# Performance work log

Measured on AMD Instinct MI355X. Metric: run time of the kernel, lower is better.

The kernel has to match this reference:

```python
import jax, jax.numpy as jnp
import numpy as np
from jax import lax

# Dims (match init_kwargs)
NP, DP = 32, 8      # num_primary_a, dim_primary_a
NT, DT = 16, 16     # num_timecaps_a, dim_timecaps
KT = 3              # kernel_timecaps_a
EPS = 1e-7


def setup_inputs() -> dict:
    key = jax.random.key(0)
    k1, k2, k3 = jax.random.split(key, 3)
    B, T = 8, 1024
    x = jax.random.normal(k1, (B, T, NP, DP), dtype=jnp.float32)
    # Conv2D kernel: HWIO = [kernel_t, dim_primary_a, in_ch=1, out_ch=NT*DT]
    conv_kernel = jax.random.normal(k2, (KT, DP, 1, NT * DT), dtype=jnp.float32) * 0.05
    conv_bias = jnp.zeros((NT * DT,), dtype=jnp.float32)
    B_weight = jax.random.normal(k3, (T, NT, 1, NP), dtype=jnp.float32) * 0.05
    return {"x": x, "conv_kernel": conv_kernel, "conv_bias": conv_bias, "B_weight": B_weight}


def reference(x, conv_kernel, conv_bias, B_weight):
    B, T, Np, Dp = x.shape
    # reshape1: [B, T, Np*Dp, 1]
    xr = x.reshape(B, T, Np * Dp, 1)
    # Conv2D(filters=NT*DT, kernel=[KT, Dp], strides=[1, Dp], padding='same', relu)
    y = lax.conv_general_dilated(
        xr, conv_kernel,
        window_strides=(1, Dp), padding='SAME',
        dimension_numbers=('NHWC', 'HWIO', 'NHWC'))
    y = jax.nn.relu(y + conv_bias)  # [B, T, Np, NT*DT]
    # reshape2 + permute -> U_hat: [B, T, NT, Np, DT]
    U = y.reshape(B, T, Np, NT, DT).transpose(0, 1, 3, 2, 4)
    # self-similarity attention
    A = jnp.einsum('btnpd,btnqd->btnpq', U, U) / jnp.sqrt(jnp.float32(Dp))
    C = jax.nn.softmax(A.sum(axis=-2, keepdims=True), axis=-1)  # [B,T,NT,1,Np]
    out = jnp.einsum('btnop,btnpd->btnod', C + B_weight, U)  # [B,T,NT,1,DT]
    out = out[..., 0, :]  # squeeze axis=-2 -> [B,T,NT,DT]
    # squash
    norm = jnp.linalg.norm(out, axis=-1, keepdims=True)
    sq = norm * norm
    return (sq / (sq + 1.0)) * (out / (norm + EPS))
```

## Files before the change

### kernel.cpp

```cpp
#include <hip/hip_runtime.h>

#define T_DIM 1024

typedef short short8 __attribute__((ext_vector_type(8)));
typedef float f32x4  __attribute__((ext_vector_type(4)));

__device__ __forceinline__ unsigned pk_bf16(float lo, float hi) {
    unsigned r;
    asm("v_cvt_pk_bf16_f32 %0, %1, %2" : "=v"(r) : "v"(lo), "v"(hi));
    return r;
}

__global__ void kpack_kernel(const float* __restrict__ K,
                             const float* __restrict__ bias,
                             uint4* __restrict__ Kp) {
    const int kb  = blockIdx.x;
    const int col = threadIdx.x;
    uint4 wv = make_uint4(0u, 0u, 0u, 0u);
    if (kb < 3) {
        const float* kp = K + kb * 8 * 256 + col;
        wv.x = pk_bf16(kp[0 * 256], kp[1 * 256]);
        wv.y = pk_bf16(kp[2 * 256], kp[3 * 256]);
        wv.z = pk_bf16(kp[4 * 256], kp[5 * 256]);
        wv.w = pk_bf16(kp[6 * 256], kp[7 * 256]);
    } else {
        wv.x = pk_bf16(bias[col], 0.f);
    }
    Kp[kb * 256 + col] = wv;
}

__device__ __forceinline__ void allred_add16_x4(float& a, float& b, float& c, float& d) {
    asm volatile(
        "s_nop 1\n\t"
        "v_add_f32_dpp %0,%0,%0 row_ror:8 row_mask:0xf bank_mask:0xf\n\t"
        "v_add_f32_dpp %1,%1,%1 row_ror:8 row_mask:0xf bank_mask:0xf\n\t"
        "v_add_f32_dpp %2,%2,%2 row_ror:8 row_mask:0xf bank_mask:0xf\n\t"
        "v_add_f32_dpp %3,%3,%3 row_ror:8 row_mask:0xf bank_mask:0xf\n\t"
        "v_add_f32_dpp %0,%0,%0 row_ror:4 row_mask:0xf bank_mask:0xf\n\t"
        "v_add_f32_dpp %1,%1,%1 row_ror:4 row_mask:0xf bank_mask:0xf\n\t"
        "v_add_f32_dpp %2,%2,%2 row_ror:4 row_mask:0xf bank_mask:0xf\n\t"
        "v_add_f32_dpp %3,%3,%3 row_ror:4 row_mask:0xf bank_mask:0xf\n\t"
        "v_add_f32_dpp %0,%0,%0 row_ror:2 row_mask:0xf bank_mask:0xf\n\t"
        "v_add_f32_dpp %1,%1,%1 row_ror:2 row_mask:0xf bank_mask:0xf\n\t"
        "v_add_f32_dpp %2,%2,%2 row_ror:2 row_mask:0xf bank_mask:0xf\n\t"
        "v_add_f32_dpp %3,%3,%3 row_ror:2 row_mask:0xf bank_mask:0xf\n\t"
        "v_add_f32_dpp %0,%0,%0 row_ror:1 row_mask:0xf bank_mask:0xf\n\t"
        "v_add_f32_dpp %1,%1,%1 row_ror:1 row_mask:0xf bank_mask:0xf\n\t"
        "v_add_f32_dpp %2,%2,%2 row_ror:1 row_mask:0xf bank_mask:0xf\n\t"
        "v_add_f32_dpp %3,%3,%3 row_ror:1 row_mask:0xf bank_mask:0xf"
        : "+v"(a), "+v"(b), "+v"(c), "+v"(d));
}
__device__ __forceinline__ void allred_add16_v4(f32x4& v) {
    float a = v[0], b = v[1], c = v[2], d = v[3];
    allred_add16_x4(a, b, c, d);
    v = (f32x4){a, b, c, d};
}
__device__ __forceinline__ float allred_add16_s(float v) {
    asm volatile(
        "s_nop 1\n\t"
        "v_add_f32_dpp %0,%0,%0 row_ror:8 row_mask:0xf bank_mask:0xf\n\t"
        "s_nop 1\n\t"
        "v_add_f32_dpp %0,%0,%0 row_ror:4 row_mask:0xf bank_mask:0xf\n\t"
        "s_nop 1\n\t"
        "v_add_f32_dpp %0,%0,%0 row_ror:2 row_mask:0xf bank_mask:0xf\n\t"
        "s_nop 1\n\t"
        "v_add_f32_dpp %0,%0,%0 row_ror:1 row_mask:0xf bank_mask:0xf"
        : "+v"(v));
    return v;
}

__device__ __forceinline__ void wave_ds_fence() {
    asm volatile("s_waitcnt lgkmcnt(0)" ::: "memory");
}

template <int CODE>
__device__ __forceinline__ float swz_xor(float v) {
    return __int_as_float(__builtin_amdgcn_ds_swizzle(__float_as_int(v), CODE));
}

#define USTRIDE 260

__global__ __launch_bounds__(256, 4) void caps_kernel(
    const float* __restrict__ x,
    const float* __restrict__ Bw,
    const uint4* __restrict__ Kp,
    float* __restrict__ out)
{
    const int bt  = blockIdx.x;
    const int t   = bt & (T_DIM - 1);
    const int tid = threadIdx.x;
    const int l   = tid & 63;
    const int w   = tid >> 6;
    const int kb  = l >> 4;
    const int r16 = l & 15;
    const int n   = tid >> 4, j = tid & 15;

    __shared__ float Urow[32 * USTRIDE];

    const float bwj0 = Bw[(size_t)t * 512 + n * 32 + j];
    const float bwj1 = Bw[(size_t)t * 512 + n * 32 + 16 + j];

    short8 bx[2];
    if (kb == 3) {
        union { short8 s; uint4 u; } one;
        one.u = make_uint4(0x00003F80u, 0u, 0u, 0u);
        bx[0] = bx[1] = one.s;
    } else {
        const int  tt    = t + kb - 1;
        const bool valid = (tt >= 0) && (tt < T_DIM);
        #pragma unroll
        for (int qt = 0; qt < 2; ++qt) {
            float4 x0 = make_float4(0.f, 0.f, 0.f, 0.f), x1 = x0;
            if (valid) {
                const float* xp = x + ((size_t)(bt + kb - 1) * 256 + (qt * 16 + r16) * 8);
                x0 = *reinterpret_cast<const float4*>(xp);
                x1 = *reinterpret_cast<const float4*>(xp + 4);
            }
            union { short8 s; uint4 u; } bu;
            bu.u.x = pk_bf16(x0.x, x0.y);
            bu.u.y = pk_bf16(x0.z, x0.w);
            bu.u.z = pk_bf16(x1.x, x1.y);
            bu.u.w = pk_bf16(x1.z, x1.w);
            bx[qt] = bu.s;
        }
    }

    short8 af[4];
    #pragma unroll
    for (int oti = 0; oti < 4; ++oti) {
        union { short8 s; uint4 u; } au;
        au.u = Kp[kb * 256 + w * 64 + oti * 16 + r16];
        af[oti] = au.s;
    }

    const f32x4 z = (f32x4){0.f, 0.f, 0.f, 0.f};
    f32x4 acc[2][4];
    #pragma unroll
    for (int qt = 0; qt < 2; ++qt)
        #pragma unroll
        for (int oti = 0; oti < 4; ++oti)
            acc[qt][oti] = __builtin_amdgcn_mfma_f32_16x16x32_bf16(
                af[oti], bx[qt], z, 0, 0, 0);

    float* wbase = &Urow[r16 * USTRIDE + w * 64 + kb * 4];
    #pragma unroll
    for (int qt = 0; qt < 2; ++qt)
        #pragma unroll
        for (int oti = 0; oti < 4; ++oti) {
            f32x4 uv;
            #pragma unroll
            for (int e = 0; e < 4; ++e)
                uv[e] = fmaxf(acc[qt][oti][e], 0.f);
            *reinterpret_cast<f32x4*>(&wbase[qt * 16 * USTRIDE + oti * 16]) = uv;
        }

    wave_ds_fence();

    const float* rbase = &Urow[j * USTRIDE + n * 16];
    f32x4 r0[4], r1[4];
    #pragma unroll
    for (int i = 0; i < 4; ++i) {
        r0[i] = *reinterpret_cast<const f32x4*>(&rbase[4 * i]);
        r1[i] = *reinterpret_cast<const f32x4*>(&rbase[16 * USTRIDE + 4 * i]);
    }

    f32x4 V[4];
    #pragma unroll
    for (int i = 0; i < 4; ++i) {
        V[i] = r0[i] + r1[i];
        allred_add16_v4(V[i]);
    }

    float s0 = 0.f, s1 = 0.f;
    #pragma unroll
    for (int i = 0; i < 4; ++i)
        #pragma unroll
        for (int c = 0; c < 4; ++c) {
            s0 = fmaf(V[i][c], r0[i][c], s0);
            s1 = fmaf(V[i][c], r1[i][c], s1);
        }

    const float C2 = 0.51011597846f;
    const float e0 = exp2f(s0 * C2), e1 = exp2f(s1 * C2);
    const float es = allred_add16_s(e0 + e1);
    const float inv = __builtin_amdgcn_rcpf(es);
    const float c0 = fmaf(e0, inv, bwj0);
    const float c1 = fmaf(e1, inv, bwj1);

    float op16[16];
    #pragma unroll
    for (int i = 0; i < 4; ++i)
        #pragma unroll
        for (int c = 0; c < 4; ++c)
            op16[4 * i + c] = fmaf(c0, r0[i][c], c1 * r1[i][c]);

    float v8[8];
    #pragma unroll
    for (int s = 0; s < 8; ++s) {
        const float keep = (j & 8) ? op16[s + 8] : op16[s];
        const float send = (j & 8) ? op16[s] : op16[s + 8];
        v8[s] = keep + swz_xor<0x201F>(send);
    }
    float v4[4];
    #pragma unroll
    for (int s = 0; s < 4; ++s) {
        const float keep = (j & 4) ? v4[0] * 0.f + ((j & 4) ? v8[s + 4] : v8[s]) : v8[s];
        (void)keep;
        const float kp = (j & 4) ? v8[s + 4] : v8[s];
        const float sd = (j & 4) ? v8[s] : v8[s + 4];
        v4[s] = kp + swz_xor<0x101F>(sd);
    }
    float v2[2];
    #pragma unroll
    for (int s = 0; s < 2; ++s) {
        const float kp = (j & 2) ? v4[s + 2] : v4[s];
        const float sd = (j & 2) ? v4[s] : v4[s + 2];
        v2[s] = kp + swz_xor<0x081F>(sd);
    }
    const float kp1 = (j & 1) ? v2[1] : v2[0];
    const float sd1 = (j & 1) ? v2[0] : v2[1];
    const float ox = kp1 + swz_xor<0x041F>(sd1);

    const float ss  = allred_add16_s(ox * ox);
    const float nrm = sqrtf(ss);
    const float res = ss * __builtin_amdgcn_rcpf(ss + 1.f) *
                      (ox * __builtin_amdgcn_rcpf(nrm + 1e-7f));

    out[(size_t)bt * 256 + tid] = res;
}

extern "C" void kernel_launch(void* const* d_in, const int* in_sizes, int n_in,
                              void* d_out, int out_size, void* d_ws, size_t ws_size,
                              hipStream_t stream) {
    const float* x    = (const float*)d_in[0];
    const float* K    = (const float*)d_in[1];
    const float* bias = (const float*)d_in[2];
    const float* Bw   = (const float*)d_in[3];
    float* out        = (float*)d_out;
    uint4* Kp         = (uint4*)d_ws;

    kpack_kernel<<<4, 256, 0, stream>>>(K, bias, Kp);

    const int B  = in_sizes[0] / (T_DIM * 32 * 8);
    const int nb = B * T_DIM;
    caps_kernel<<<nb, 256, 0, stream>>>(x, Bw, Kp, out);
}
```

Baseline: 33.81 us.

## Fuse weight packing into caps kernel and compute column sums before LDS

Drops the separate kernel that packed conv weights to bf16 and has each block load and convert the fp32 weights itself, which removes one launch and the dependency between kernels. The column sum V is now computed right after the MFMA from the accumulators, using DPP reductions, and written to a small shared array instead of being recomputed from LDS reads by every thread. In exchange, each block performs redundant scalar global loads and conversions of the weights, which add load latency at kernel start. It also adds an extra shared buffer.

Measured after the change: 37.82 us. 11.8% more time.

```diff
diff --git a/kernel.cpp b/kernel.cpp
--- a/kernel.cpp
+++ b/kernel.cpp
@@ -9,24 +9,6 @@
     unsigned r;
     asm("v_cvt_pk_bf16_f32 %0, %1, %2" : "=v"(r) : "v"(lo), "v"(hi));
     return r;
-}
-
-__global__ void kpack_kernel(const float* __restrict__ K,
-                             const float* __restrict__ bias,
-                             uint4* __restrict__ Kp) {
-    const int kb  = blockIdx.x;
-    const int col = threadIdx.x;
-    uint4 wv = make_uint4(0u, 0u, 0u, 0u);
-    if (kb < 3) {
-        const float* kp = K + kb * 8 * 256 + col;
-        wv.x = pk_bf16(kp[0 * 256], kp[1 * 256]);
-        wv.y = pk_bf16(kp[2 * 256], kp[3 * 256]);
-        wv.z = pk_bf16(kp[4 * 256], kp[5 * 256]);
-        wv.w = pk_bf16(kp[6 * 256], kp[7 * 256]);
-    } else {
-        wv.x = pk_bf16(bias[col], 0.f);
-    }
-    Kp[kb * 256 + col] = wv;
 }
 
 __device__ __forceinline__ void allred_add16_x4(float& a, float& b, float& c, float& d) {
@@ -50,11 +32,6 @@
         "v_add_f32_dpp %3,%3,%3 row_ror:1 row_mask:0xf bank_mask:0xf"
         : "+v"(a), "+v"(b), "+v"(c), "+v"(d));
 }
-__device__ __forceinline__ void allred_add16_v4(f32x4& v) {
-    float a = v[0], b = v[1], c = v[2], d = v[3];
-    allred_add16_x4(a, b, c, d);
-    v = (f32x4){a, b, c, d};
-}
 __device__ __forceinline__ float allred_add16_s(float v) {
     asm volatile(
         "s_nop 1\n\t"
@@ -83,7 +60,8 @@
 __global__ __launch_bounds__(256, 4) void caps_kernel(
     const float* __restrict__ x,
     const float* __restrict__ Bw,
-    const uint4* __restrict__ Kp,
+    const float* __restrict__ K,
+    const float* __restrict__ bias,
     float* __restrict__ out)
 {
     const int bt  = blockIdx.x;
@@ -96,6 +74,7 @@
     const int n   = tid >> 4, j = tid & 15;
 
     __shared__ float Urow[32 * USTRIDE];
+    __shared__ float Vs[256];
 
     const float bwj0 = Bw[(size_t)t * 512 + n * 32 + j];
     const float bwj1 = Bw[(size_t)t * 512 + n * 32 + 16 + j];
@@ -128,8 +107,17 @@
     short8 af[4];
     #pragma unroll
     for (int oti = 0; oti < 4; ++oti) {
+        const int col = w * 64 + oti * 16 + r16;
         union { short8 s; uint4 u; } au;
-        au.u = Kp[kb * 256 + w * 64 + oti * 16 + r16];
+        if (kb < 3) {
+            const float* kp = K + (kb * 8) * 256 + col;
+            au.u.x = pk_bf16(kp[0 * 256], kp[1 * 256]);
+            au.u.y = pk_bf16(kp[2 * 256], kp[3 * 256]);
+            au.u.z = pk_bf16(kp[4 * 256], kp[5 * 256]);
+            au.u.w = pk_bf16(kp[6 * 256], kp[7 * 256]);
+        } else {
+            au.u = make_uint4(pk_bf16(bias[col], 0.f), 0u, 0u, 0u);
+        }
         af[oti] = au.s;
     }
 
@@ -144,31 +132,33 @@
 
     float* wbase = &Urow[r16 * USTRIDE + w * 64 + kb * 4];
     #pragma unroll
-    for (int qt = 0; qt < 2; ++qt)
-        #pragma unroll
-        for (int oti = 0; oti < 4; ++oti) {
-            f32x4 uv;
-            #pragma unroll
-            for (int e = 0; e < 4; ++e)
-                uv[e] = fmaxf(acc[qt][oti][e], 0.f);
-            *reinterpret_cast<f32x4*>(&wbase[qt * 16 * USTRIDE + oti * 16]) = uv;
-        }
+    for (int oti = 0; oti < 4; ++oti) {
+        f32x4 uv0, uv1;
+        #pragma unroll
+        for (int e = 0; e < 4; ++e) {
+            uv0[e] = fmaxf(acc[0][oti][e], 0.f);
+            uv1[e] = fmaxf(acc[1][oti][e], 0.f);
+        }
+        *reinterpret_cast<f32x4*>(&wbase[oti * 16]) = uv0;
+        *reinterpret_cast<f32x4*>(&wbase[16 * USTRIDE + oti * 16]) = uv1;
+
+        float v0 = uv0[0] + uv1[0], v1 = uv0[1] + uv1[1];
+        float v2 = uv0[2] + uv1[2], v3 = uv0[3] + uv1[3];
+        allred_add16_x4(v0, v1, v2, v3);
+        if (r16 == 0)
+            *reinterpret_cast<f32x4*>(&Vs[w * 64 + oti * 16 + kb * 4]) =
+                (f32x4){v0, v1, v2, v3};
+    }
 
     wave_ds_fence();
 
     const float* rbase = &Urow[j * USTRIDE + n * 16];
-    f32x4 r0[4], r1[4];
+    f32x4 r0[4], r1[4], V[4];
     #pragma unroll
     for (int i = 0; i < 4; ++i) {
         r0[i] = *reinterpret_cast<const f32x4*>(&rbase[4 * i]);
         r1[i] = *reinterpret_cast<const f32x4*>(&rbase[16 * USTRIDE + 4 * i]);
-    }
-
-    f32x4 V[4];
-    #pragma unroll
-    for (int i = 0; i < 4; ++i) {
-        V[i] = r0[i] + r1[i];
-        allred_add16_v4(V[i]);
+        V[i]  = *reinterpret_cast<const f32x4*>(&Vs[n * 16 + 4 * i]);
     }
 
     float s0 = 0.f, s1 = 0.f;
@@ -197,15 +187,13 @@
     float v8[8];
     #pragma unroll
     for (int s = 0; s < 8; ++s) {
-        const float keep = (j & 8) ? op16[s + 8] : op16[s];
-        const float send = (j & 8) ? op16[s] : op16[s + 8];
-        v8[s] = keep + swz_xor<0x201F>(send);
+        const float kp = (j & 8) ? op16[s + 8] : op16[s];
+        const float sd = (j & 8) ? op16[s] : op16[s + 8];
+        v8[s] = kp + swz_xor<0x201F>(sd);
     }
     float v4[4];
     #pragma unroll
     for (int s = 0; s < 4; ++s) {
-        const float keep = (j & 4) ? v4[0] * 0.f + ((j & 4) ? v8[s + 4] : v8[s]) : v8[s];
-        (void)keep;
         const float kp = (j & 4) ? v8[s + 4] : v8[s];
         const float sd = (j & 4) ? v8[s] : v8[s + 4];
         v4[s] = kp + swz_xor<0x101F>(sd);
@@ -237,11 +225,8 @@
     const float* bias = (const float*)d_in[2];
     const float* Bw   = (const float*)d_in[3];
     float* out        = (float*)d_out;
-    uint4* Kp         = (uint4*)d_ws;
-
-    kpack_kernel<<<4, 256, 0, stream>>>(K, bias, Kp);
 
     const int B  = in_sizes[0] / (T_DIM * 32 * 8);
     const int nb = B * T_DIM;
-    caps_kernel<<<nb, 256, 0, stream>>>(x, Bw, Kp, out);
-}
+    caps_kernel<<<nb, 256, 0, stream>>>(x, Bw, K, bias, out);
+}
```

## Compute capsule attention directly in MFMA register layout, dropping LDS staging

Applied to the files above, without the earlier changes.

Removes the shared-memory round trip that transposed the MFMA output into a per-thread row layout. The similarity, softmax, weighted sum and squash are now computed in the MFMA accumulator layout, using DPP row reductions plus cross-row shuffles. Occupancy in the launch bounds rises from 4 to 5 now that LDS is gone. The cost is more cross-lane reduction work per output capsule, and only one lane in sixteen issues each float4 store.

After: 39.91 us. 1.18x slower.

```diff
diff --git a/kernel.cpp b/kernel.cpp
--- a/kernel.cpp
+++ b/kernel.cpp
@@ -50,11 +50,6 @@
         "v_add_f32_dpp %3,%3,%3 row_ror:1 row_mask:0xf bank_mask:0xf"
         : "+v"(a), "+v"(b), "+v"(c), "+v"(d));
 }
-__device__ __forceinline__ void allred_add16_v4(f32x4& v) {
-    float a = v[0], b = v[1], c = v[2], d = v[3];
-    allred_add16_x4(a, b, c, d);
-    v = (f32x4){a, b, c, d};
-}
 __device__ __forceinline__ float allred_add16_s(float v) {
     asm volatile(
         "s_nop 1\n\t"
@@ -69,18 +64,7 @@
     return v;
 }
 
-__device__ __forceinline__ void wave_ds_fence() {
-    asm volatile("s_waitcnt lgkmcnt(0)" ::: "memory");
-}
-
-template <int CODE>
-__device__ __forceinline__ float swz_xor(float v) {
-    return __int_as_float(__builtin_amdgcn_ds_swizzle(__float_as_int(v), CODE));
-}
-
-#define USTRIDE 260
-
-__global__ __launch_bounds__(256, 4) void caps_kernel(
+__global__ __launch_bounds__(256, 5) void caps_kernel(
     const float* __restrict__ x,
     const float* __restrict__ Bw,
     const uint4* __restrict__ Kp,
@@ -93,12 +77,15 @@
     const int w   = tid >> 6;
     const int kb  = l >> 4;
     const int r16 = l & 15;
-    const int n   = tid >> 4, j = tid & 15;
 
-    __shared__ float Urow[32 * USTRIDE];
-
-    const float bwj0 = Bw[(size_t)t * 512 + n * 32 + j];
-    const float bwj1 = Bw[(size_t)t * 512 + n * 32 + 16 + j];
+    float bwq0[4], bwq1[4];
+    const float* bwt = Bw + (size_t)t * 512;
+    #pragma unroll
+    for (int oti = 0; oti < 4; ++oti) {
+        const int h = w * 4 + oti;
+        bwq0[oti] = bwt[h * 32 + r16];
+        bwq1[oti] = bwt[h * 32 + 16 + r16];
+    }
 
     short8 bx[2];
     if (kb == 3) {
@@ -142,91 +129,52 @@
             acc[qt][oti] = __builtin_amdgcn_mfma_f32_16x16x32_bf16(
                 af[oti], bx[qt], z, 0, 0, 0);
 
-    float* wbase = &Urow[r16 * USTRIDE + w * 64 + kb * 4];
+    const float C2 = 0.51011597846f;
     #pragma unroll
-    for (int qt = 0; qt < 2; ++qt)
+    for (int oti = 0; oti < 4; ++oti) {
+        const int h = w * 4 + oti;
+
+        float u0[4], u1[4];
         #pragma unroll
-        for (int oti = 0; oti < 4; ++oti) {
-            f32x4 uv;
-            #pragma unroll
-            for (int e = 0; e < 4; ++e)
-                uv[e] = fmaxf(acc[qt][oti][e], 0.f);
-            *reinterpret_cast<f32x4*>(&wbase[qt * 16 * USTRIDE + oti * 16]) = uv;
+        for (int e = 0; e < 4; ++e) {
+            u0[e] = fmaxf(acc[0][oti][e], 0.f);
+            u1[e] = fmaxf(acc[1][oti][e], 0.f);
         }
 
-    wave_ds_fence();
+        float v0 = u0[0] + u1[0], v1 = u0[1] + u1[1];
+        float v2 = u0[2] + u1[2], v3 = u0[3] + u1[3];
+        allred_add16_x4(v0, v1, v2, v3);
 
-    const float* rbase = &Urow[j * USTRIDE + n * 16];
-    f32x4 r0[4], r1[4];
-    #pragma unroll
-    for (int i = 0; i < 4; ++i) {
-        r0[i] = *reinterpret_cast<const f32x4*>(&rbase[4 * i]);
-        r1[i] = *reinterpret_cast<const f32x4*>(&rbase[16 * USTRIDE + 4 * i]);
+        float s0 = v0 * u0[0] + v1 * u0[1] + v2 * u0[2] + v3 * u0[3];
+        float s1 = v0 * u1[0] + v1 * u1[1] + v2 * u1[2] + v3 * u1[3];
+        s0 += __shfl_xor(s0, 16);  s0 += __shfl_xor(s0, 32);
+        s1 += __shfl_xor(s1, 16);  s1 += __shfl_xor(s1, 32);
+
+        const float e0 = exp2f(s0 * C2), e1 = exp2f(s1 * C2);
+        const float es = allred_add16_s(e0 + e1);
+        const float inv = __builtin_amdgcn_rcpf(es);
+        const float c0 = fmaf(e0, inv, bwq0[oti]);
+        const float c1 = fmaf(e1, inv, bwq1[oti]);
+
+        float o0 = c0 * u0[0] + c1 * u1[0];
+        float o1 = c0 * u0[1] + c1 * u1[1];
+        float o2 = c0 * u0[2] + c1 * u1[2];
+        float o3 = c0 * u0[3] + c1 * u1[3];
+        allred_add16_x4(o0, o1, o2, o3);
+
+        float ss = o0 * o0 + o1 * o1 + o2 * o2 + o3 * o3;
+        ss += __shfl_xor(ss, 16);
+        ss += __shfl_xor(ss, 32);
+
+        const float nrm = sqrtf(ss);
+        const float g = ss * __builtin_amdgcn_rcpf(ss + 1.f) *
+                        __builtin_amdgcn_rcpf(nrm + 1e-7f);
+
+        if (r16 == 0) {
+            float4 res = make_float4(o0 * g, o1 * g, o2 * g, o3 * g);
+            *reinterpret_cast<float4*>(&out[(size_t)bt * 256 + h * 16 + kb * 4]) = res;
+        }
     }
-
-    f32x4 V[4];
-    #pragma unroll
-    for (int i = 0; i < 4; ++i) {
-        V[i] = r0[i] + r1[i];
-        allred_add16_v4(V[i]);
-    }
-
-    float s0 = 0.f, s1 = 0.f;
-    #pragma unroll
-    for (int i = 0; i < 4; ++i)
-        #pragma unroll
-        for (int c = 0; c < 4; ++c) {
-            s0 = fmaf(V[i][c], r0[i][c], s0);
-            s1 = fmaf(V[i][c], r1[i][c], s1);
-        }
-
-    const float C2 = 0.51011597846f;
-    const float e0 = exp2f(s0 * C2), e1 = exp2f(s1 * C2);
-    const float es = allred_add16_s(e0 + e1);
-    const float inv = __builtin_amdgcn_rcpf(es);
-    const float c0 = fmaf(e0, inv, bwj0);
-    const float c1 = fmaf(e1, inv, bwj1);
-
-    float op16[16];
-    #pragma unroll
-    for (int i = 0; i < 4; ++i)
-        #pragma unroll
-        for (int c = 0; c < 4; ++c)
-            op16[4 * i + c] = fmaf(c0, r0[i][c], c1 * r1[i][c]);
-
-    float v8[8];
-    #pragma unroll
-    for (int s = 0; s < 8; ++s) {
-        const float keep = (j & 8) ? op16[s + 8] : op16[s];
-        const float send = (j & 8) ? op16[s] : op16[s + 8];
-        v8[s] = keep + swz_xor<0x201F>(send);
-    }
-    float v4[4];
-    #pragma unroll
-    for (int s = 0; s < 4; ++s) {
-        const float keep = (j & 4) ? v4[0] * 0.f + ((j & 4) ? v8[s + 4] : v8[s]) : v8[s];
-        (void)keep;
-        const float kp = (j & 4) ? v8[s + 4] : v8[s];
-        const float sd = (j & 4) ? v8[s] : v8[s + 4];
-        v4[s] = kp + swz_xor<0x101F>(sd);
-    }
-    float v2[2];
-    #pragma unroll
-    for (int s = 0; s < 2; ++s) {
-        const float kp = (j & 2) ? v4[s + 2] : v4[s];
-        const float sd = (j & 2) ? v4[s] : v4[s + 2];
-        v2[s] = kp + swz_xor<0x081F>(sd);
-    }
-    const float kp1 = (j & 1) ? v2[1] : v2[0];
-    const float sd1 = (j & 1) ? v2[0] : v2[1];
-    const float ox = kp1 + swz_xor<0x041F>(sd1);
-
-    const float ss  = allred_add16_s(ox * ox);
-    const float nrm = sqrtf(ss);
-    const float res = ss * __builtin_amdgcn_rcpf(ss + 1.f) *
-                      (ox * __builtin_amdgcn_rcpf(nrm + 1e-7f));
-
-    out[(size_t)bt * 256 + tid] = res;
 }
 
 extern "C" void kernel_launch(void* const* d_in, const int* in_sizes, int n_in,
```

## Store conv output as bf16 in XOR-swizzled LDS and raise occupancy

Applied to the files above, without the earlier changes.

The intermediate U tile in shared memory is now stored as packed bf16 instead of fp32, and the padded layout is replaced by an XOR-swizzled index so writes and reads avoid bank conflicts. This halves LDS usage per block (16KB instead of about 33KB), and launch bounds are raised from 4 to 8 blocks per CU to exploit the extra room. The cost is more rounding in the attention and weighted-sum stages, plus unpack shifts on every read.

Result: faster. 32.61 us, median of 2 (-3.6%).

```diff
diff --git a/kernel.cpp b/kernel.cpp
--- a/kernel.cpp
+++ b/kernel.cpp
@@ -29,6 +29,19 @@
     Kp[kb * 256 + col] = wv;
 }
 
+__device__ __forceinline__ float allred_add16_s(float v) {
+    asm volatile(
+        "s_nop 1\n\t"
+        "v_add_f32_dpp %0,%0,%0 row_ror:8 row_mask:0xf bank_mask:0xf\n\t"
+        "s_nop 1\n\t"
+        "v_add_f32_dpp %0,%0,%0 row_ror:4 row_mask:0xf bank_mask:0xf\n\t"
+        "s_nop 1\n\t"
+        "v_add_f32_dpp %0,%0,%0 row_ror:2 row_mask:0xf bank_mask:0xf\n\t"
+        "s_nop 1\n\t"
+        "v_add_f32_dpp %0,%0,%0 row_ror:1 row_mask:0xf bank_mask:0xf"
+        : "+v"(v));
+    return v;
+}
 __device__ __forceinline__ void allred_add16_x4(float& a, float& b, float& c, float& d) {
     asm volatile(
         "s_nop 1\n\t"
@@ -50,24 +63,6 @@
         "v_add_f32_dpp %3,%3,%3 row_ror:1 row_mask:0xf bank_mask:0xf"
         : "+v"(a), "+v"(b), "+v"(c), "+v"(d));
 }
-__device__ __forceinline__ void allred_add16_v4(f32x4& v) {
-    float a = v[0], b = v[1], c = v[2], d = v[3];
-    allred_add16_x4(a, b, c, d);
-    v = (f32x4){a, b, c, d};
-}
-__device__ __forceinline__ float allred_add16_s(float v) {
-    asm volatile(
-        "s_nop 1\n\t"
-        "v_add_f32_dpp %0,%0,%0 row_ror:8 row_mask:0xf bank_mask:0xf\n\t"
-        "s_nop 1\n\t"
-        "v_add_f32_dpp %0,%0,%0 row_ror:4 row_mask:0xf bank_mask:0xf\n\t"
-        "s_nop 1\n\t"
-        "v_add_f32_dpp %0,%0,%0 row_ror:2 row_mask:0xf bank_mask:0xf\n\t"
-        "s_nop 1\n\t"
-        "v_add_f32_dpp %0,%0,%0 row_ror:1 row_mask:0xf bank_mask:0xf"
-        : "+v"(v));
-    return v;
-}
 
 __device__ __forceinline__ void wave_ds_fence() {
     asm volatile("s_waitcnt lgkmcnt(0)" ::: "memory");
@@ -78,9 +73,13 @@
     return __int_as_float(__builtin_amdgcn_ds_swizzle(__float_as_int(v), CODE));
 }
 
-#define USTRIDE 260
-
-__global__ __launch_bounds__(256, 4) void caps_kernel(
+__device__ __forceinline__ int sidx(int q, int o) {
+    return q * 256 + ((((o >> 2) ^ (q & 15)) << 2) | (o & 3));
+}
+__device__ __forceinline__ float bf_lo(unsigned u) { return __uint_as_float(u << 16); }
+__device__ __forceinline__ float bf_hi(unsigned u) { return __uint_as_float(u & 0xffff0000u); }
+
+__global__ __launch_bounds__(256, 8) void caps_kernel(
     const float* __restrict__ x,
     const float* __restrict__ Bw,
     const uint4* __restrict__ Kp,
@@ -95,7 +94,7 @@
     const int r16 = l & 15;
     const int n   = tid >> 4, j = tid & 15;
 
-    __shared__ float Urow[32 * USTRIDE];
+    __shared__ unsigned short U16[32 * 256];
 
     const float bwj0 = Bw[(size_t)t * 512 + n * 32 + j];
     const float bwj1 = Bw[(size_t)t * 512 + n * 32 + 16 + j];
@@ -142,33 +141,37 @@
             acc[qt][oti] = __builtin_amdgcn_mfma_f32_16x16x32_bf16(
                 af[oti], bx[qt], z, 0, 0, 0);
 
-    float* wbase = &Urow[r16 * USTRIDE + w * 64 + kb * 4];
-    #pragma unroll
-    for (int qt = 0; qt < 2; ++qt)
+    #pragma unroll
+    for (int qt = 0; qt < 2; ++qt) {
+        const int q = qt * 16 + r16;
         #pragma unroll
         for (int oti = 0; oti < 4; ++oti) {
-            f32x4 uv;
-            #pragma unroll
-            for (int e = 0; e < 4; ++e)
-                uv[e] = fmaxf(acc[qt][oti][e], 0.f);
-            *reinterpret_cast<f32x4*>(&wbase[qt * 16 * USTRIDE + oti * 16]) = uv;
+            const int obase = w * 64 + oti * 16 + kb * 4;
+            uint2 pk;
+            pk.x = pk_bf16(fmaxf(acc[qt][oti][0], 0.f), fmaxf(acc[qt][oti][1], 0.f));
+            pk.y = pk_bf16(fmaxf(acc[qt][oti][2], 0.f), fmaxf(acc[qt][oti][3], 0.f));
+            *reinterpret_cast<uint2*>(&U16[sidx(q, obase)]) = pk;
         }
+    }
 
     wave_ds_fence();
 
-    const float* rbase = &Urow[j * USTRIDE + n * 16];
     f32x4 r0[4], r1[4];
     #pragma unroll
     for (int i = 0; i < 4; ++i) {
-        r0[i] = *reinterpret_cast<const f32x4*>(&rbase[4 * i]);
-        r1[i] = *reinterpret_cast<const f32x4*>(&rbase[16 * USTRIDE + 4 * i]);
+        const uint2 a = *reinterpret_cast<const uint2*>(&U16[sidx(j,      n * 16 + 4 * i)]);
+        const uint2 c = *reinterpret_cast<const uint2*>(&U16[sidx(j + 16, n * 16 + 4 * i)]);
+        r0[i] = (f32x4){bf_lo(a.x), bf_hi(a.x), bf_lo(a.y), bf_hi(a.y)};
+        r1[i] = (f32x4){bf_lo(c.x), bf_hi(c.x), bf_lo(c.y), bf_hi(c.y)};
     }
 
     f32x4 V[4];
     #pragma unroll
     for (int i = 0; i < 4; ++i) {
         V[i] = r0[i] + r1[i];
-        allred_add16_v4(V[i]);
+        float a = V[i][0], b = V[i][1], c = V[i][2], d = V[i][3];
+        allred_add16_x4(a, b, c, d);
+        V[i] = (f32x4){a, b, c, d};
     }
 
     float s0 = 0.f, s1 = 0.f;
@@ -197,15 +200,13 @@
     float v8[8];
     #pragma unroll
     for (int s = 0; s < 8; ++s) {
-        const float keep = (j & 8) ? op16[s + 8] : op16[s];
-        const float send = (j & 8) ? op16[s] : op16[s + 8];
-        v8[s] = keep + swz_xor<0x201F>(send);
+        const float kp = (j & 8) ? op16[s + 8] : op16[s];
+        const float sd = (j & 8) ? op16[s] : op16[s + 8];
+        v8[s] = kp + swz_xor<0x201F>(sd);
     }
     float v4[4];
     #pragma unroll
     for (int s = 0; s < 4; ++s) {
-        const float keep = (j & 4) ? v4[0] * 0.f + ((j & 4) ? v8[s + 4] : v8[s]) : v8[s];
-        (void)keep;
         const float kp = (j & 4) ? v8[s + 4] : v8[s];
         const float sd = (j & 4) ? v8[s] : v8[s + 4];
         v4[s] = kp + swz_xor<0x101F>(sd);
```
